# Kernel tuning notes

Measured on AMD Instinct MI355X. Metric: run time of the kernel, lower is better.

## Reference

```python
import jax, jax.numpy as jnp
import numpy as np

C = 128          # channel_size
H = 2            # num_head
HD = C // H      # per-head dim = 64
SCALE = C ** 0.5 # note: module scales by sqrt(channel_size), not sqrt(head_dim)


def setup_inputs() -> dict:
    key = jax.random.key(0)
    k_x, k_w, k_b = jax.random.split(key, 3)
    x = jax.random.normal(k_x, (8, 64, 256, C), dtype=jnp.float32)
    # nn.Linear(C, 3C): weight [3C, C], bias [3C]; y = x @ W.T + b
    bound = 1.0 / np.sqrt(C)
    W_qkv = jax.random.uniform(k_w, (3 * C, C), dtype=jnp.float32, minval=-bound, maxval=bound)
    b_qkv = jax.random.uniform(k_b, (3 * C,), dtype=jnp.float32, minval=-bound, maxval=bound)
    return {"x": x, "W_qkv": W_qkv, "b_qkv": b_qkv}


def reference(x, W_qkv, b_qkv):
    b, l, g, _ = x.shape
    qkv = jnp.einsum('blgc,dc->blgd', x, W_qkv) + b_qkv        # [b,l,g,3C]
    # rearrange 'b l g (d h c) -> d b l h g c'
    qkv = qkv.reshape(b, l, g, 3, H, HD)
    qkv = jnp.transpose(qkv, (3, 0, 1, 4, 2, 5))               # [3,b,l,h,g,c]
    q, k, v = qkv[0], qkv[1], qkv[2]
    score = jnp.einsum('blhgc,blhkc->blhgk', q, k) / SCALE      # [b,l,h,g,g]
    score = jax.nn.softmax(score, axis=-1)
    out = jnp.einsum('blhgk,blhkc->blhgc', score, v)            # [b,l,h,g,c]
    # rearrange 'b l h g c -> b l g (h c)'
    out = jnp.transpose(out, (0, 1, 3, 2, 4)).reshape(b, l, g, H * HD)
    return out
```

## Files before the change

### kernel.cpp

```cpp
#include <hip/hip_runtime.h>
#include <hip/hip_bf16.h>


typedef __bf16 bf16x8 __attribute__((ext_vector_type(8)));
typedef float  f32x4  __attribute__((ext_vector_type(4)));
typedef float  f32x16 __attribute__((ext_vector_type(16)));

#define MFMA16(a, b, c) __builtin_amdgcn_mfma_f32_16x16x32_bf16((a), (b), (c), 0, 0, 0)
#define MFMA32(a, b, c) __builtin_amdgcn_mfma_f32_32x32x16_bf16((a), (b), (c), 0, 0, 0)

namespace dmsa {

constexpr int G  = 256;
constexpr int C  = 128;
constexpr int HD = 64;
constexpr float QSCALE = 1.4426950408889634f * 0.08838834764831845f;

__device__ __forceinline__ unsigned pack2(float a, float b) {
    union { __hip_bfloat162 h; unsigned u; } c;
    c.h = __float22bfloat162_rn(make_float2(a, b));
    return c.u;
}
__device__ __forceinline__ uint2 pack4(float a, float b, float c, float d) {
    uint2 r; r.x = pack2(a, b); r.y = pack2(c, d); return r;
}
__device__ __forceinline__ uint4 pack8(const float* p) {
    uint4 r;
    r.x = pack2(p[0], p[1]); r.y = pack2(p[2], p[3]);
    r.z = pack2(p[4], p[5]); r.w = pack2(p[6], p[7]);
    return r;
}
__device__ __forceinline__ bf16x8 lds8(const ushort* p) { return *(const bf16x8*)p; }
__device__ __forceinline__ bf16x8 ldg8(const ushort* p) { return *(const bf16x8*)p; }
__device__ __forceinline__ bf16x8 ld8f(const float* __restrict__ p) {
    float t[8];
    *(float4*)t       = *(const float4*)p;
    *(float4*)(t + 4) = *(const float4*)(p + 4);
    union { uint4 u; bf16x8 v; } c;
    c.u = pack8(t);
    return c.v;
}

__global__ void convw(const float* __restrict__ W, ushort* __restrict__ wbf) {
    int t = blockIdx.x * 256 + threadIdx.x;
    float tmp[8];
    const float* p = W + (size_t)t * 8;
    *(float4*)tmp       = *(const float4*)p;
    *(float4*)(tmp + 4) = *(const float4*)(p + 4);
    *(uint4*)(wbf + (size_t)t * 8) = pack8(tmp);
}

__global__ __launch_bounds__(256, 2)
void fused(const float* __restrict__ x, const ushort* __restrict__ wb,
           const float* __restrict__ bias, float* __restrict__ out)
{
    __shared__ ushort kc[G * 72];
    __shared__ ushort vc[HD * 264];

    const int tid = threadIdx.x, wv = tid >> 6, lane = tid & 63;
    const int l16 = lane & 15, quad = lane >> 4;
    const int l32 = lane & 31, hl = lane >> 5;

    const int b  = blockIdx.x;
    const int L  = ((b & 7) << 7) | (b >> 3);
    const int bl = L >> 1, h = L & 1;

    const float*  xr = x  + (size_t)bl * G * C;
    const ushort* Wq = wb + (size_t)(h * HD) * C;
    const ushort* Wk = wb + (size_t)(C + h * HD) * C;
    const ushort* Wv = wb + (size_t)(2 * C + h * HD) * C;

    const int r0 = wv * 64;
    const f32x4 z4 = {0.f, 0.f, 0.f, 0.f};

    bf16x8 xf[4][4];
    #pragma unroll
    for (int i = 0; i < 4; ++i)
        #pragma unroll
        for (int kk = 0; kk < 4; ++kk)
            xf[i][kk] = ld8f(xr + (size_t)(r0 + i * 16 + l16) * C + kk * 32 + quad * 8);

    f32x4 qacc[4][4];
    #pragma unroll
    for (int mi = 0; mi < 4; ++mi)
        #pragma unroll
        for (int ni = 0; ni < 4; ++ni) qacc[mi][ni] = z4;
    #pragma unroll
    for (int kk = 0; kk < 4; ++kk)
        #pragma unroll
        for (int mi = 0; mi < 4; ++mi) {
            bf16x8 a = ldg8(Wq + (size_t)(mi * 16 + l16) * C + kk * 32 + quad * 8);
            #pragma unroll
            for (int ni = 0; ni < 4; ++ni)
                qacc[mi][ni] = MFMA16(a, xf[ni][kk], qacc[mi][ni]);
        }
    ushort* qs = kc + r0 * 72;
    #pragma unroll
    for (int mi = 0; mi < 4; ++mi) {
        float4 bs = *(const float4*)(bias + h * HD + mi * 16 + quad * 4);
        #pragma unroll
        for (int ni = 0; ni < 4; ++ni)
            *(uint2*)(qs + (ni * 16 + l16) * 72 + mi * 16 + quad * 4) =
                pack4((qacc[mi][ni][0] + bs.x) * QSCALE,
                      (qacc[mi][ni][1] + bs.y) * QSCALE,
                      (qacc[mi][ni][2] + bs.z) * QSCALE,
                      (qacc[mi][ni][3] + bs.w) * QSCALE);
    }
    bf16x8 qf[2][4];
    #pragma unroll
    for (int ni = 0; ni < 2; ++ni)
        #pragma unroll
        for (int kk = 0; kk < 4; ++kk)
            qf[ni][kk] = lds8(qs + (ni * 32 + l32) * 72 + kk * 16 + hl * 8);

    {
        f32x4 kacc[4][4];
        #pragma unroll
        for (int mi = 0; mi < 4; ++mi)
            #pragma unroll
            for (int nt = 0; nt < 4; ++nt) kacc[mi][nt] = z4;
        #pragma unroll
        for (int kk = 0; kk < 4; ++kk)
            #pragma unroll
            for (int mi = 0; mi < 4; ++mi) {
                bf16x8 a = ldg8(Wk + (size_t)(mi * 16 + l16) * C + kk * 32 + quad * 8);
                #pragma unroll
                for (int nt = 0; nt < 4; ++nt)
                    kacc[mi][nt] = MFMA16(a, xf[nt][kk], kacc[mi][nt]);
            }
        #pragma unroll
        for (int mi = 0; mi < 4; ++mi) {
            float4 bs = *(const float4*)(bias + C + h * HD + mi * 16 + quad * 4);
            #pragma unroll
            for (int nt = 0; nt < 4; ++nt)
                *(uint2*)(kc + (r0 + nt * 16 + l16) * 72 + mi * 16 + quad * 4) =
                    pack4(kacc[mi][nt][0] + bs.x, kacc[mi][nt][1] + bs.y,
                          kacc[mi][nt][2] + bs.z, kacc[mi][nt][3] + bs.w);
        }
    }

    {
        f32x4 vacc[4][4];
        #pragma unroll
        for (int mt = 0; mt < 4; ++mt)
            #pragma unroll
            for (int nt = 0; nt < 4; ++nt) vacc[mt][nt] = z4;
        #pragma unroll
        for (int kk = 0; kk < 4; ++kk)
            #pragma unroll
            for (int nt = 0; nt < 4; ++nt) {
                bf16x8 bw = ldg8(Wv + (size_t)(nt * 16 + l16) * C + kk * 32 + quad * 8);
                #pragma unroll
                for (int mt = 0; mt < 4; ++mt)
                    vacc[mt][nt] = MFMA16(xf[mt][kk], bw, vacc[mt][nt]);
            }
        #pragma unroll
        for (int nt = 0; nt < 4; ++nt) {
            float bv = bias[2 * C + h * HD + nt * 16 + l16];
            #pragma unroll
            for (int mt = 0; mt < 4; ++mt)
                *(uint2*)(vc + (nt * 16 + l16) * 264 + r0 + mt * 16 + quad * 4) =
                    pack4(vacc[mt][nt][0] + bv, vacc[mt][nt][1] + bv,
                          vacc[mt][nt][2] + bv, vacc[mt][nt][3] + bv);
        }
    }

    __syncthreads();

    float lacc[2] = {0.f, 0.f};
    f32x16 oacc[2][2];
    #pragma unroll
    for (int mt = 0; mt < 2; ++mt)
        #pragma unroll
        for (int ni = 0; ni < 2; ++ni)
            #pragma unroll
            for (int r = 0; r < 16; ++r) oacc[mt][ni][r] = 0.f;

    const int spoff = 2 * wv + ((b & 1) << 2);

    #pragma unroll 2
    for (int sp = 0; sp < 8; ++sp) {
        const int g0 = ((sp + spoff) & 7) * 32;

        bf16x8 kf[4];
        #pragma unroll
        for (int kk = 0; kk < 4; ++kk)
            kf[kk] = lds8(kc + (g0 + l32) * 72 + kk * 16 + hl * 8);
        bf16x8 vf[2][2];
        #pragma unroll
        for (int mt = 0; mt < 2; ++mt)
            #pragma unroll
            for (int ch = 0; ch < 2; ++ch)
                vf[mt][ch] = lds8(vc + (mt * 32 + l32) * 264 + g0 + ch * 16 + hl * 8);

        #pragma unroll
        for (int ni = 0; ni < 2; ++ni) {
            f32x16 s;
            #pragma unroll
            for (int r = 0; r < 16; ++r) s[r] = 0.f;
            __builtin_amdgcn_s_setprio(1);
            #pragma unroll
            for (int kk = 0; kk < 4; ++kk)
                s = MFMA32(kf[kk], qf[ni][kk], s);
            __builtin_amdgcn_s_setprio(0);

            float part = 0.f;
            #pragma unroll
            for (int r = 0; r < 16; ++r) {
                float p = __builtin_amdgcn_exp2f(s[r]);
                s[r] = p;
                part += p;
            }
            lacc[ni] += part;

            #pragma unroll
            for (int ch = 0; ch < 2; ++ch) {
                unsigned p0a = pack2(s[8 * ch + 0], s[8 * ch + 1]);
                unsigned p0b = pack2(s[8 * ch + 2], s[8 * ch + 3]);
                unsigned p1a = pack2(s[8 * ch + 4], s[8 * ch + 5]);
                unsigned p1b = pack2(s[8 * ch + 6], s[8 * ch + 7]);
                auto w02 = __builtin_amdgcn_permlane32_swap((int)p0a, (int)p1a, false, false);
                auto w13 = __builtin_amdgcn_permlane32_swap((int)p0b, (int)p1b, false, false);
                union { uint4 u; bf16x8 v; } pf;
                pf.u.x = (unsigned)w02[0]; pf.u.y = (unsigned)w13[0];
                pf.u.z = (unsigned)w02[1]; pf.u.w = (unsigned)w13[1];
                __builtin_amdgcn_s_setprio(1);
                #pragma unroll
                for (int mt = 0; mt < 2; ++mt)
                    oacc[mt][ni] = MFMA32(vf[mt][ch], pf.v, oacc[mt][ni]);
                __builtin_amdgcn_s_setprio(0);
            }
        }
    }

    float* og = out + (size_t)bl * G * C + h * HD;
    #pragma unroll
    for (int ni = 0; ni < 2; ++ni) {
        float l = lacc[ni];
        l += __shfl_xor(l, 32);
        float inv = 1.0f / l;
        int g = r0 + ni * 32 + l32;
        #pragma unroll
        for (int mt = 0; mt < 2; ++mt)
            #pragma unroll
            for (int rr = 0; rr < 4; ++rr) {
                float4 st;
                st.x = oacc[mt][ni][4 * rr + 0] * inv;
                st.y = oacc[mt][ni][4 * rr + 1] * inv;
                st.z = oacc[mt][ni][4 * rr + 2] * inv;
                st.w = oacc[mt][ni][4 * rr + 3] * inv;
                *(float4*)(og + (size_t)g * C + mt * 32 + rr * 8 + hl * 4) = st;
            }
    }
}

}

extern "C" void kernel_launch(void* const* d_in, const int* in_sizes, int n_in,
                              void* d_out, int out_size, void* d_ws, size_t ws_size,
                              hipStream_t stream) {
    (void)in_sizes; (void)n_in; (void)out_size;

    if (ws_size < (size_t)384 * 128 * 2) return;

    const float* x    = (const float*)d_in[0];
    const float* W    = (const float*)d_in[1];
    const float* bias = (const float*)d_in[2];
    float* out = (float*)d_out;

    ushort* wbf = (ushort*)d_ws;

    dmsa::convw<<<dim3(24),   dim3(256), 0, stream>>>(W, wbf);
    dmsa::fused<<<dim3(1024), dim3(256), 0, stream>>>(x, wbf, bias, out);
}
```

Baseline: 158.3 us.

## Double-buffer K/V LDS fragments and interleave both query tiles per strip

Restructures the attention inner loop so the K and V register fragments for the next key strip are loaded from LDS while the current strip's softmax and PV MFMAs run, using ping-pong register buffers. It also issues both query-tile QK MFMA chains back to back before the exponentials, and computes the row sum as a tree instead of a serial chain. The aim is to hide LDS read latency and give the scheduler more independent MFMA work. The cost is extra live registers for the second fragment set, which may reduce occupancy or cause spills.

```diff
diff --git a/kernel.cpp b/kernel.cpp
--- a/kernel.cpp
+++ b/kernel.cpp
@@ -178,59 +178,78 @@
 
     const int spoff = 2 * wv + ((b & 1) << 2);
 
-    #pragma unroll 2
-    for (int sp = 0; sp < 8; ++sp) {
-        const int g0 = ((sp + spoff) & 7) * 32;
-
-        bf16x8 kf[4];
+    bf16x8 kfA[4], vfA[4], kfB[4], vfB[4];
+
+    auto ldkv = [&](bf16x8 (&kf)[4], bf16x8 (&vf)[4], int g0) {
         #pragma unroll
         for (int kk = 0; kk < 4; ++kk)
             kf[kk] = lds8(kc + (g0 + l32) * 72 + kk * 16 + hl * 8);
-        bf16x8 vf[2][2];
         #pragma unroll
         for (int mt = 0; mt < 2; ++mt)
             #pragma unroll
             for (int ch = 0; ch < 2; ++ch)
-                vf[mt][ch] = lds8(vc + (mt * 32 + l32) * 264 + g0 + ch * 16 + hl * 8);
-
-        #pragma unroll
-        for (int ni = 0; ni < 2; ++ni) {
-            f32x16 s;
-            #pragma unroll
-            for (int r = 0; r < 16; ++r) s[r] = 0.f;
-            __builtin_amdgcn_s_setprio(1);
-            #pragma unroll
-            for (int kk = 0; kk < 4; ++kk)
-                s = MFMA32(kf[kk], qf[ni][kk], s);
-            __builtin_amdgcn_s_setprio(0);
-
-            float part = 0.f;
-            #pragma unroll
-            for (int r = 0; r < 16; ++r) {
-                float p = __builtin_amdgcn_exp2f(s[r]);
-                s[r] = p;
-                part += p;
-            }
-            lacc[ni] += part;
-
-            #pragma unroll
-            for (int ch = 0; ch < 2; ++ch) {
-                unsigned p0a = pack2(s[8 * ch + 0], s[8 * ch + 1]);
-                unsigned p0b = pack2(s[8 * ch + 2], s[8 * ch + 3]);
-                unsigned p1a = pack2(s[8 * ch + 4], s[8 * ch + 5]);
-                unsigned p1b = pack2(s[8 * ch + 6], s[8 * ch + 7]);
-                auto w02 = __builtin_amdgcn_permlane32_swap((int)p0a, (int)p1a, false, false);
-                auto w13 = __builtin_amdgcn_permlane32_swap((int)p0b, (int)p1b, false, false);
-                union { uint4 u; bf16x8 v; } pf;
-                pf.u.x = (unsigned)w02[0]; pf.u.y = (unsigned)w13[0];
-                pf.u.z = (unsigned)w02[1]; pf.u.w = (unsigned)w13[1];
-                __builtin_amdgcn_s_setprio(1);
-                #pragma unroll
-                for (int mt = 0; mt < 2; ++mt)
-                    oacc[mt][ni] = MFMA32(vf[mt][ch], pf.v, oacc[mt][ni]);
-                __builtin_amdgcn_s_setprio(0);
-            }
-        }
+                vf[mt * 2 + ch] = lds8(vc + (mt * 32 + l32) * 264 + g0 + ch * 16 + hl * 8);
+    };
+
+    auto smx = [&](f32x16& s, float& lsum, bf16x8& pa, bf16x8& pb) {
+        #pragma unroll
+        for (int r = 0; r < 16; ++r) s[r] = __builtin_amdgcn_exp2f(s[r]);
+        float a0 = (s[0] + s[1]) + (s[2] + s[3]);
+        float a1 = (s[4] + s[5]) + (s[6] + s[7]);
+        float a2 = (s[8] + s[9]) + (s[10] + s[11]);
+        float a3 = (s[12] + s[13]) + (s[14] + s[15]);
+        lsum += (a0 + a1) + (a2 + a3);
+        #pragma unroll
+        for (int ch = 0; ch < 2; ++ch) {
+            unsigned p0a = pack2(s[8 * ch + 0], s[8 * ch + 1]);
+            unsigned p0b = pack2(s[8 * ch + 2], s[8 * ch + 3]);
+            unsigned p1a = pack2(s[8 * ch + 4], s[8 * ch + 5]);
+            unsigned p1b = pack2(s[8 * ch + 6], s[8 * ch + 7]);
+            auto w02 = __builtin_amdgcn_permlane32_swap((int)p0a, (int)p1a, false, false);
+            auto w13 = __builtin_amdgcn_permlane32_swap((int)p0b, (int)p1b, false, false);
+            union { uint4 u; bf16x8 v; } pf_;
+            pf_.u.x = (unsigned)w02[0]; pf_.u.y = (unsigned)w13[0];
+            pf_.u.z = (unsigned)w02[1]; pf_.u.w = (unsigned)w13[1];
+            if (ch == 0) pa = pf_.v; else pb = pf_.v;
+        }
+    };
+
+    auto strip = [&](bf16x8 (&kfC)[4], bf16x8 (&vfC)[4],
+                     bf16x8 (&kfN)[4], bf16x8 (&vfN)[4],
+                     int g0, int gn, bool pf) {
+        f32x16 s0, s1;
+        #pragma unroll
+        for (int r = 0; r < 16; ++r) { s0[r] = 0.f; s1[r] = 0.f; }
+        __builtin_amdgcn_s_setprio(1);
+        #pragma unroll
+        for (int kk = 0; kk < 4; ++kk) s0 = MFMA32(kfC[kk], qf[0][kk], s0);
+        #pragma unroll
+        for (int kk = 0; kk < 4; ++kk) s1 = MFMA32(kfC[kk], qf[1][kk], s1);
+        __builtin_amdgcn_s_setprio(0);
+        if (pf) ldkv(kfN, vfN, gn);
+        bf16x8 p0a, p0b, p1a, p1b;
+        smx(s0, lacc[0], p0a, p0b);
+        smx(s1, lacc[1], p1a, p1b);
+        __builtin_amdgcn_s_setprio(1);
+        oacc[0][0] = MFMA32(vfC[0], p0a, oacc[0][0]);
+        oacc[0][0] = MFMA32(vfC[1], p0b, oacc[0][0]);
+        oacc[1][0] = MFMA32(vfC[2], p0a, oacc[1][0]);
+        oacc[1][0] = MFMA32(vfC[3], p0b, oacc[1][0]);
+        oacc[0][1] = MFMA32(vfC[0], p1a, oacc[0][1]);
+        oacc[0][1] = MFMA32(vfC[1], p1b, oacc[0][1]);
+        oacc[1][1] = MFMA32(vfC[2], p1a, oacc[1][1]);
+        oacc[1][1] = MFMA32(vfC[3], p1b, oacc[1][1]);
+        __builtin_amdgcn_s_setprio(0);
+    };
+
+    ldkv(kfA, vfA, (spoff & 7) * 32);
+    #pragma unroll 1
+    for (int it = 0; it < 4; ++it) {
+        const int t = 2 * it;
+        strip(kfA, vfA, kfB, vfB,
+              ((spoff + t) & 7) * 32, ((spoff + t + 1) & 7) * 32, true);
+        strip(kfB, vfB, kfA, vfA,
+              ((spoff + t + 1) & 7) * 32, ((spoff + t + 2) & 7) * 32, it < 3);
     }
 
     float* og = out + (size_t)bl * G * C + h * HD;
```

Result: no change. 160.8 us (+1.6%).
